# Kernel optimization log

Hardware: AMD Instinct MI355X
Metric: run time of the kernel (lower is better)

Reference implementation:

```python
import jax, jax.numpy as jnp
import numpy as np

B = 512          # batch
T_STEPS = 32     # clip_length (loop runs T-1 = 32 times)
BELIEF = 1024
STATE = 256
HIDDEN = 1024
EMB = 1024
POSE_TILES = 1
MIN_STD = 0.1


def setup_inputs() -> dict:
    key = jax.random.key(0)
    ks = jax.random.split(key, 24)
    s = 0.02
    rn = lambda k, sh: (jax.random.normal(k, sh, dtype=jnp.float32) * s)
    d = {
        "prev_state": jax.random.normal(ks[0], (B, STATE), dtype=jnp.float32),
        "prev_belief": jax.random.normal(ks[1], (B, BELIEF), dtype=jnp.float32),
        "poses": jax.random.normal(ks[2], (T_STEPS, B, 6), dtype=jnp.float32),
        "observations": jax.random.normal(ks[3], (T_STEPS, B, EMB), dtype=jnp.float32),
        "post_noise": jax.random.normal(ks[4], (T_STEPS, B, STATE), dtype=jnp.float32),
        "prior_noise": jax.random.normal(ks[5], (T_STEPS, B, STATE), dtype=jnp.float32),
        # fc_embed_state: 2*state -> belief
        "w_es": rn(ks[6], (2 * STATE, BELIEF)), "b_es": jnp.zeros((BELIEF,), jnp.float32),
        # GRUCell(belief, belief); torch gate order r, z, n
        "w_ih": rn(ks[7], (BELIEF, 3 * BELIEF)), "w_hh": rn(ks[8], (BELIEF, 3 * BELIEF)),
        "b_ih": jnp.zeros((3 * BELIEF,), jnp.float32), "b_hh": jnp.zeros((3 * BELIEF,), jnp.float32),
        # fc_embed_belief_posterior: belief+emb -> hidden
        "w_ebpo": rn(ks[9], (BELIEF + EMB, HIDDEN)), "b_ebpo": jnp.zeros((HIDDEN,), jnp.float32),
        # fc_state_posterior: hidden -> 2*state
        "w_spo": rn(ks[10], (HIDDEN, 2 * STATE)), "b_spo": jnp.zeros((2 * STATE,), jnp.float32),
        # fc_embed_belief_prior: belief + 6*pose_tiles -> hidden
        "w_ebpr": rn(ks[11], (BELIEF + 6 * POSE_TILES, HIDDEN)), "b_ebpr": jnp.zeros((HIDDEN,), jnp.float32),
        # fc_state_prior: hidden -> 2*state
        "w_spr": rn(ks[12], (HIDDEN, 2 * STATE)), "b_spr": jnp.zeros((2 * STATE,), jnp.float32),
    }
    return d


def _rssm(prev_state, prev_belief, poses, observations, post_noise, prior_noise,
          w_es, b_es, w_ih, w_hh, b_ih, b_hh,
          w_ebpo, b_ebpo, w_spo, b_spo, w_ebpr, b_ebpr, w_spr, b_spr):
    def gru_cell(x, h):
        gi = x @ w_ih + b_ih
        gh = h @ w_hh + b_hh
        ir, iz, inn = jnp.split(gi, 3, axis=1)
        hr, hz, hn = jnp.split(gh, 3, axis=1)
        r = jax.nn.sigmoid(ir + hr)
        z = jax.nn.sigmoid(iz + hz)
        n = jnp.tanh(inn + r * hn)
        return (1.0 - z) * n + z * h

    def step(carry, xs):
        post_s, prior_s, belief = carry
        obs_t, pose_t, n_post, n_prior = xs
        hidden = jax.nn.relu(jnp.concatenate([post_s, prior_s], axis=1) @ w_es + b_es)
        belief = gru_cell(hidden, belief)
        # posterior branch
        hp = jax.nn.relu(jnp.concatenate([belief, obs_t], axis=1) @ w_ebpo + b_ebpo)
        pm, psd_raw = jnp.split(hp @ w_spo + b_spo, 2, axis=1)
        psd = jax.nn.softplus(psd_raw) + MIN_STD
        ps = pm + psd * n_post
        # prior branch (pose tiled)
        pose_rep = jnp.tile(pose_t, (1, POSE_TILES))
        hq = jax.nn.relu(jnp.concatenate([belief, pose_rep], axis=1) @ w_ebpr + b_ebpr)
        prm, prsd_raw = jnp.split(hq @ w_spr + b_spr, 2, axis=1)
        prsd = jax.nn.softplus(prsd_raw) + MIN_STD
        prs = prm + prsd * n_prior
        return (ps, prs, belief), (belief, prs, prm, prsd, ps, pm, psd)

    init = (prev_state, prev_state, prev_belief)
    _, outs = jax.lax.scan(step, init, (observations, poses, post_noise, prior_noise))
    # outs: beliefs, prior_states, prior_means, prior_std_devs, posterior_states, posterior_means, posterior_std_devs  (each [T-1, B, *])
    return outs


def reference(prev_state, prev_belief, poses, observations, post_noise, prior_noise,
              w_es, b_es, w_ih, w_hh, b_ih, b_hh,
              w_ebpo, b_ebpo, w_spo, b_spo, w_ebpr, b_ebpr, w_spr, b_spr):
    return _rssm(prev_state, prev_belief, poses, observations, post_noise, prior_noise,
                 w_es, b_es, w_ih, w_hh, b_ih, b_hh,
                 w_ebpo, b_ebpo, w_spo, b_spo, w_ebpr, b_ebpr, w_spr, b_spr)
```

## Files before the change

kernel.cpp:

```cpp
#include <hip/hip_runtime.h>
#include <math.h>


typedef __attribute__((ext_vector_type(8))) short bf16x8;
typedef __attribute__((ext_vector_type(4))) float f32x4;

#define MFMA(a, b, c) __builtin_amdgcn_mfma_f32_16x16x32_bf16(a, b, c, 0, 0, 0)

__device__ __forceinline__ short f2bf(float f) {
    unsigned u = __float_as_uint(f);
    u += 0x7FFF + ((u >> 16) & 1);
    return (short)(u >> 16);
}
__device__ __forceinline__ float sigmoidf_(float x) { return 1.f / (1.f + expf(-x)); }
__device__ __forceinline__ float softplusf_(float x) {
    return fmaxf(x, 0.f) + log1pf(expf(-fabsf(x)));
}
__device__ __forceinline__ f32x4 zero4() { f32x4 v = {0.f, 0.f, 0.f, 0.f}; return v; }

__global__ __launch_bounds__(256) void k_swizzle(const float* __restrict__ W,
                                                 short* __restrict__ out,
                                                 int KT, int N)
{
    int gw = blockIdx.x * 4 + (threadIdx.x >> 6);
    int lane = threadIdx.x & 63;
    int nt = gw / KT, kt = gw % KT;
    const float* src = W + (size_t)(kt * 32 + (lane >> 4) * 8) * N + nt * 16 + (lane & 15);
    short tmp[8];
#pragma unroll
    for (int j = 0; j < 8; ++j) tmp[j] = f2bf(src[(size_t)j * N]);
    *(bf16x8*)(out + (((size_t)gw * 64 + lane) << 3)) = *(const bf16x8*)tmp;
}

__global__ __launch_bounds__(256) void k_obs2bf(const float* __restrict__ obs,
                                                short* __restrict__ out)
{
    size_t i = ((size_t)blockIdx.x * 256 + threadIdx.x) * 8;
    short tmp[8];
#pragma unroll
    for (int j = 0; j < 8; ++j) tmp[j] = f2bf(obs[i + j]);
    *(bf16x8*)(out + i) = *(const bf16x8*)tmp;
}

__global__ __launch_bounds__(256) void k_init(const float* __restrict__ prev_state,
                                              const float* __restrict__ prev_belief,
                                              short* __restrict__ stateCat,
                                              short* __restrict__ belief1)
{
    int i = blockIdx.x * 256 + threadIdx.x;
    if (i < 262144) {
        int m = i >> 9, c = i & 511;
        stateCat[i] = f2bf(prev_state[m * 256 + (c & 255)]);
    } else {
        int j = i - 262144;
        belief1[j] = f2bf(prev_belief[j]);
    }
}

__device__ __forceinline__ bf16x8 loadA16(const short* A, int m0, int kelem, int strideElems, int lane) {
    return *(const bf16x8*)(A + (size_t)(m0 + (lane & 15)) * strideElems + kelem + ((lane >> 4) << 3));
}
__device__ __forceinline__ bf16x8 loadB16(const short* Bsw, size_t tileIdx, int lane) {
    return *(const bf16x8*)(Bsw + ((tileIdx * 64 + lane) << 3));
}

__global__ __launch_bounds__(256) void k_embed_state(
    const short* __restrict__ A, const short* __restrict__ Bsw,
    const float* __restrict__ bias, short* __restrict__ outBf)
{
    int wid = threadIdx.x >> 6;
    int lane = threadIdx.x & 63;
    int nt = blockIdx.x & 63, mb = blockIdx.x >> 6;
    int m0 = (mb * 4 + wid) * 32;
    f32x4 acc0 = zero4(), acc1 = zero4();
#pragma unroll 4
    for (int kt = 0; kt < 16; ++kt) {
        bf16x8 a0 = loadA16(A, m0,      kt * 32, 512, lane);
        bf16x8 a1 = loadA16(A, m0 + 16, kt * 32, 512, lane);
        bf16x8 b  = loadB16(Bsw, (size_t)nt * 16 + kt, lane);
        acc0 = MFMA(a0, b, acc0);
        acc1 = MFMA(a1, b, acc1);
    }
    int q = lane >> 4, cl = lane & 15;
    int n = nt * 16 + cl;
    float bn = bias[n];
#pragma unroll
    for (int i = 0; i < 4; ++i) {
        int m = m0 + q * 4 + i;
        outBf[(size_t)m * 1024 + n]        = f2bf(fmaxf(acc0[i] + bn, 0.f));
        outBf[(size_t)(m + 16) * 1024 + n] = f2bf(fmaxf(acc1[i] + bn, 0.f));
    }
}

__global__ __launch_bounds__(256) void k_gru(
    const short* __restrict__ Hbf, const short* __restrict__ Pbf,
    const float* __restrict__ Pf32,
    const short* __restrict__ sw_ih, const short* __restrict__ sw_hh,
    const float* __restrict__ b_ih, const float* __restrict__ b_hh,
    float* __restrict__ belF32, short* __restrict__ belBf)
{
    int wid = threadIdx.x >> 6;
    int lane = threadIdx.x & 63;
    int nt = blockIdx.x & 63, mb = blockIdx.x >> 6;
    int m0 = (mb * 4 + wid) * 32;
    f32x4 r0 = zero4(), r1 = zero4(), z0 = zero4(), z1 = zero4();
    f32x4 ni0 = zero4(), ni1 = zero4(), nh0 = zero4(), nh1 = zero4();

#pragma unroll 4
    for (int kt = 0; kt < 32; ++kt) {
        bf16x8 a0 = loadA16(Hbf, m0,      kt * 32, 1024, lane);
        bf16x8 a1 = loadA16(Hbf, m0 + 16, kt * 32, 1024, lane);
        bf16x8 br = loadB16(sw_ih, (size_t)(0 * 64 + nt) * 32 + kt, lane);
        bf16x8 bz = loadB16(sw_ih, (size_t)(1 * 64 + nt) * 32 + kt, lane);
        bf16x8 bn = loadB16(sw_ih, (size_t)(2 * 64 + nt) * 32 + kt, lane);
        r0 = MFMA(a0, br, r0);   r1 = MFMA(a1, br, r1);
        z0 = MFMA(a0, bz, z0);   z1 = MFMA(a1, bz, z1);
        ni0 = MFMA(a0, bn, ni0); ni1 = MFMA(a1, bn, ni1);
    }
#pragma unroll 4
    for (int kt = 0; kt < 32; ++kt) {
        bf16x8 a0 = loadA16(Pbf, m0,      kt * 32, 1024, lane);
        bf16x8 a1 = loadA16(Pbf, m0 + 16, kt * 32, 1024, lane);
        bf16x8 br = loadB16(sw_hh, (size_t)(0 * 64 + nt) * 32 + kt, lane);
        bf16x8 bz = loadB16(sw_hh, (size_t)(1 * 64 + nt) * 32 + kt, lane);
        bf16x8 bn = loadB16(sw_hh, (size_t)(2 * 64 + nt) * 32 + kt, lane);
        r0 = MFMA(a0, br, r0);   r1 = MFMA(a1, br, r1);
        z0 = MFMA(a0, bz, z0);   z1 = MFMA(a1, bz, z1);
        nh0 = MFMA(a0, bn, nh0); nh1 = MFMA(a1, bn, nh1);
    }

    int q = lane >> 4, cl = lane & 15;
    int n = nt * 16 + cl;
    float bihr = b_ih[n] + b_hh[n];
    float bihz = b_ih[1024 + n] + b_hh[1024 + n];
    float bin = b_ih[2048 + n], bhn = b_hh[2048 + n];
#pragma unroll
    for (int f = 0; f < 2; ++f) {
#pragma unroll
        for (int i = 0; i < 4; ++i) {
            int m = m0 + f * 16 + q * 4 + i;
            float rv = f ? r1[i] : r0[i];
            float zv = f ? z1[i] : z0[i];
            float niv = f ? ni1[i] : ni0[i];
            float nhv = f ? nh1[i] : nh0[i];
            float rr = sigmoidf_(rv + bihr);
            float zz = sigmoidf_(zv + bihz);
            float ng = tanhf(niv + bin + rr * (nhv + bhn));
            float h = Pf32[(size_t)m * 1024 + n];
            float v = (1.f - zz) * ng + zz * h;
            belF32[(size_t)m * 1024 + n] = v;
            belBf[(size_t)m * 1024 + n] = f2bf(v);
        }
    }
}

__global__ __launch_bounds__(256) void k_pp(
    const short* __restrict__ Bel, const short* __restrict__ ObsBf,
    const float* __restrict__ Pose,
    const short* __restrict__ sw_ebpo, const short* __restrict__ sw_ebpr,
    const float* __restrict__ Wf_ebpr,
    const float* __restrict__ b_ebpo, const float* __restrict__ b_ebpr,
    short* __restrict__ hpBf, short* __restrict__ hqBf)
{
    int wid = threadIdx.x >> 6;
    int lane = threadIdx.x & 63;
    int q = lane >> 4, cl = lane & 15;
    int b = blockIdx.x;
    if (b < 256) {
        int nt = b & 63, mb = b >> 6;
        int m0 = (mb * 4 + wid) * 32;
        f32x4 acc0 = zero4(), acc1 = zero4();
#pragma unroll 4
        for (int kt = 0; kt < 32; ++kt) {
            bf16x8 a0 = loadA16(Bel, m0,      kt * 32, 1024, lane);
            bf16x8 a1 = loadA16(Bel, m0 + 16, kt * 32, 1024, lane);
            bf16x8 bb = loadB16(sw_ebpo, (size_t)nt * 64 + kt, lane);
            acc0 = MFMA(a0, bb, acc0);
            acc1 = MFMA(a1, bb, acc1);
        }
#pragma unroll 4
        for (int kt = 32; kt < 64; ++kt) {
            bf16x8 a0 = loadA16(ObsBf, m0,      (kt - 32) * 32, 1024, lane);
            bf16x8 a1 = loadA16(ObsBf, m0 + 16, (kt - 32) * 32, 1024, lane);
            bf16x8 bb = loadB16(sw_ebpo, (size_t)nt * 64 + kt, lane);
            acc0 = MFMA(a0, bb, acc0);
            acc1 = MFMA(a1, bb, acc1);
        }
        int n = nt * 16 + cl;
        float bn = b_ebpo[n];
#pragma unroll
        for (int i = 0; i < 4; ++i) {
            int m = m0 + q * 4 + i;
            hpBf[(size_t)m * 1024 + n]        = f2bf(fmaxf(acc0[i] + bn, 0.f));
            hpBf[(size_t)(m + 16) * 1024 + n] = f2bf(fmaxf(acc1[i] + bn, 0.f));
        }
    } else {
        int b2 = b - 256;
        int nt = b2 & 63, mb = b2 >> 6;
        int m0 = (mb * 4 + wid) * 32;
        f32x4 acc0 = zero4(), acc1 = zero4();
#pragma unroll 4
        for (int kt = 0; kt < 32; ++kt) {
            bf16x8 a0 = loadA16(Bel, m0,      kt * 32, 1024, lane);
            bf16x8 a1 = loadA16(Bel, m0 + 16, kt * 32, 1024, lane);
            bf16x8 bb = loadB16(sw_ebpr, (size_t)nt * 32 + kt, lane);
            acc0 = MFMA(a0, bb, acc0);
            acc1 = MFMA(a1, bb, acc1);
        }
        int n = nt * 16 + cl;
        float bn = b_ebpr[n];
#pragma unroll
        for (int f = 0; f < 2; ++f) {
#pragma unroll
            for (int i = 0; i < 4; ++i) {
                int m = m0 + f * 16 + q * 4 + i;
                float v = (f ? acc1[i] : acc0[i]) + bn;
#pragma unroll
                for (int p = 0; p < 6; ++p)
                    v += Pose[(size_t)m * 6 + p] * Wf_ebpr[(size_t)(1024 + p) * 1024 + n];
                hqBf[(size_t)m * 1024 + n] = f2bf(fmaxf(v, 0.f));
            }
        }
    }
}

__global__ __launch_bounds__(256) void k_head(
    const short* __restrict__ Hp, const short* __restrict__ Hq,
    const short* __restrict__ sw_spo, const short* __restrict__ sw_spr,
    const float* __restrict__ b_spo, const float* __restrict__ b_spr,
    const float* __restrict__ nPost, const float* __restrict__ nPri,
    float* __restrict__ pM, float* __restrict__ pS, float* __restrict__ pSt,
    float* __restrict__ qM, float* __restrict__ qS, float* __restrict__ qSt,
    short* __restrict__ stateCat)
{
    int gw = blockIdx.x * 4 + (threadIdx.x >> 6);
    int lane = threadIdx.x & 63;
    int br = gw >> 9, rem = gw & 511;
    int mt = rem >> 4, ct = rem & 15;
    int m0 = mt * 16;
    const short* A = br ? Hq : Hp;
    const short* Bsw = br ? sw_spr : sw_spo;
    const float* bias = br ? b_spr : b_spo;
    const float* noise = br ? nPri : nPost;
    float* mO = br ? qM : pM;
    float* sO = br ? qS : pS;
    float* stO = br ? qSt : pSt;
    int catOff = br ? 256 : 0;
    f32x4 ma = zero4(), sa = zero4();
#pragma unroll 4
    for (int kt = 0; kt < 32; ++kt) {
        bf16x8 a = loadA16(A, m0, kt * 32, 1024, lane);
        bf16x8 bm = loadB16(Bsw, (size_t)ct * 32 + kt, lane);
        bf16x8 bs = loadB16(Bsw, (size_t)(16 + ct) * 32 + kt, lane);
        ma = MFMA(a, bm, ma);
        sa = MFMA(a, bs, sa);
    }
    int q = lane >> 4, cl = lane & 15;
#pragma unroll
    for (int i = 0; i < 4; ++i) {
        int m = m0 + q * 4 + i;
        int c = ct * 16 + cl;
        float mean = ma[i] + bias[c];
        float sd = softplusf_(sa[i] + bias[c + 256]) + 0.1f;
        float st = mean + sd * noise[(size_t)m * 256 + c];
        mO[(size_t)m * 256 + c] = mean;
        sO[(size_t)m * 256 + c] = sd;
        stO[(size_t)m * 256 + c] = st;
        stateCat[(size_t)m * 512 + catOff + c] = f2bf(st);
    }
}

extern "C" void kernel_launch(void* const* d_in, const int* in_sizes, int n_in,
                              void* d_out, int out_size, void* d_ws, size_t ws_size,
                              hipStream_t stream)
{
    const float* prev_state  = (const float*)d_in[0];
    const float* prev_belief = (const float*)d_in[1];
    const float* poses       = (const float*)d_in[2];
    const float* obs         = (const float*)d_in[3];
    const float* post_noise  = (const float*)d_in[4];
    const float* prior_noise = (const float*)d_in[5];
    const float* w_es   = (const float*)d_in[6];
    const float* b_es   = (const float*)d_in[7];
    const float* w_ih   = (const float*)d_in[8];
    const float* w_hh   = (const float*)d_in[9];
    const float* b_ih   = (const float*)d_in[10];
    const float* b_hh   = (const float*)d_in[11];
    const float* w_ebpo = (const float*)d_in[12];
    const float* b_ebpo = (const float*)d_in[13];
    const float* w_spo  = (const float*)d_in[14];
    const float* b_spo  = (const float*)d_in[15];
    const float* w_ebpr = (const float*)d_in[16];
    const float* b_ebpr = (const float*)d_in[17];
    const float* w_spr  = (const float*)d_in[18];
    const float* b_spr  = (const float*)d_in[19];

    float* out = (float*)d_out;
    float* beliefs    = out;
    float* priStates  = out + 16777216;
    float* priMeans   = out + 20971520;
    float* priStds    = out + 25165824;
    float* postStates = out + 29360128;
    float* postMeans  = out + 33554432;
    float* postStds   = out + 37748736;

    short* ws = (short*)d_ws;
    size_t o = 0;
    short* sw_es   = ws + o; o += (size_t)512 * 1024;
    short* sw_ih   = ws + o; o += (size_t)1024 * 3072;
    short* sw_hh   = ws + o; o += (size_t)1024 * 3072;
    short* sw_ebpo = ws + o; o += (size_t)2048 * 1024;
    short* sw_ebpr = ws + o; o += (size_t)1024 * 1024;
    short* sw_spo  = ws + o; o += (size_t)1024 * 512;
    short* sw_spr  = ws + o; o += (size_t)1024 * 512;
    short* hidden  = ws + o; o += (size_t)512 * 1024;
    short* belBuf0 = ws + o; o += (size_t)512 * 1024;
    short* belBuf1 = ws + o; o += (size_t)512 * 1024;
    short* hpBuf   = ws + o; o += (size_t)512 * 1024;
    short* hqBuf   = ws + o; o += (size_t)512 * 1024;
    short* stateCat = ws + o; o += (size_t)512 * 512;
    short* obsBf   = ws + o; o += (size_t)32 * 512 * 1024;

    k_swizzle<<<dim3(256),  dim3(256), 0, stream>>>(w_es,   sw_es,   16, 1024);
    k_swizzle<<<dim3(1536), dim3(256), 0, stream>>>(w_ih,   sw_ih,   32, 3072);
    k_swizzle<<<dim3(1536), dim3(256), 0, stream>>>(w_hh,   sw_hh,   32, 3072);
    k_swizzle<<<dim3(1024), dim3(256), 0, stream>>>(w_ebpo, sw_ebpo, 64, 1024);
    k_swizzle<<<dim3(512),  dim3(256), 0, stream>>>(w_ebpr, sw_ebpr, 32, 1024);
    k_swizzle<<<dim3(256),  dim3(256), 0, stream>>>(w_spo,  sw_spo,  32, 512);
    k_swizzle<<<dim3(256),  dim3(256), 0, stream>>>(w_spr,  sw_spr,  32, 512);
    k_obs2bf<<<dim3(8192), dim3(256), 0, stream>>>(obs, obsBf);
    k_init<<<dim3(3072), dim3(256), 0, stream>>>(prev_state, prev_belief, stateCat, belBuf1);

    for (int t = 0; t < 32; ++t) {
        short* belPrevBf = (t & 1) ? belBuf0 : belBuf1;
        short* belCurBf  = (t & 1) ? belBuf1 : belBuf0;
        const float* belPrevF = t ? (beliefs + (size_t)(t - 1) * 524288) : prev_belief;
        float* belT = beliefs + (size_t)t * 524288;

        k_embed_state<<<dim3(256), dim3(256), 0, stream>>>(stateCat, sw_es, b_es, hidden);
        k_gru<<<dim3(256), dim3(256), 0, stream>>>(hidden, belPrevBf, belPrevF,
                                                   sw_ih, sw_hh, b_ih, b_hh, belT, belCurBf);
        k_pp<<<dim3(512), dim3(256), 0, stream>>>(belCurBf, obsBf + (size_t)t * 524288,
                                                  poses + (size_t)t * 3072,
                                                  sw_ebpo, sw_ebpr, w_ebpr,
                                                  b_ebpo, b_ebpr, hpBuf, hqBuf);
        k_head<<<dim3(256), dim3(256), 0, stream>>>(hpBuf, hqBuf, sw_spo, sw_spr, b_spo, b_spr,
                                                    post_noise + (size_t)t * 131072,
                                                    prior_noise + (size_t)t * 131072,
                                                    postMeans + (size_t)t * 131072,
                                                    postStds + (size_t)t * 131072,
                                                    postStates + (size_t)t * 131072,
                                                    priMeans + (size_t)t * 131072,
                                                    priStds + (size_t)t * 131072,
                                                    priStates + (size_t)t * 131072,
                                                    stateCat);
    }
}
```

Baseline: 2.693 ms.

## Fuse per-step kernels into one persistent cooperative kernel with grid barriers

Replaces the 128 per-timestep kernel launches with a single cooperative persistent kernel of 256 blocks. It loops over time steps and separates the embed, GRU, posterior/prior hidden and head phases with a software global barrier built on atomics. This removes launch and drain overhead between dependent phases. The trade-off is that the k_pp phase, which previously used 512 blocks, now runs serially within 256 blocks, and the spin barriers add their own latency. The old multi-launch path is kept as a fallback if the cooperative launch fails.

```diff
diff --git a/kernel.cpp b/kernel.cpp
--- a/kernel.cpp
+++ b/kernel.cpp
@@ -45,9 +45,11 @@
 __global__ __launch_bounds__(256) void k_init(const float* __restrict__ prev_state,
                                               const float* __restrict__ prev_belief,
                                               short* __restrict__ stateCat,
-                                              short* __restrict__ belief1)
+                                              short* __restrict__ belief1,
+                                              unsigned* __restrict__ bar)
 {
     int i = blockIdx.x * 256 + threadIdx.x;
+    if (i == 0) { bar[0] = 0u; bar[1] = 0u; }
     if (i < 262144) {
         int m = i >> 9, c = i & 511;
         stateCat[i] = f2bf(prev_state[m * 256 + (c & 255)]);
@@ -64,6 +66,215 @@
     return *(const bf16x8*)(Bsw + ((tileIdx * 64 + lane) << 3));
 }
 
+#define NBLK 256
+
+__device__ __forceinline__ void gbar(unsigned* bar)
+{
+    __syncthreads();
+    if (threadIdx.x == 0) {
+        __threadfence();
+        unsigned g = __hip_atomic_load(bar + 1, __ATOMIC_RELAXED, __HIP_MEMORY_SCOPE_AGENT);
+        unsigned a = __hip_atomic_fetch_add(bar, 1u, __ATOMIC_ACQ_REL, __HIP_MEMORY_SCOPE_AGENT);
+        if (a == NBLK - 1) {
+            __hip_atomic_store(bar, 0u, __ATOMIC_RELAXED, __HIP_MEMORY_SCOPE_AGENT);
+            __hip_atomic_fetch_add(bar + 1, 1u, __ATOMIC_RELEASE, __HIP_MEMORY_SCOPE_AGENT);
+        } else {
+            while (__hip_atomic_load(bar + 1, __ATOMIC_ACQUIRE, __HIP_MEMORY_SCOPE_AGENT) == g)
+                __builtin_amdgcn_s_sleep(2);
+        }
+        __threadfence();
+    }
+    __syncthreads();
+}
+
+struct RP {
+    const short *sw_es, *sw_ih, *sw_hh, *sw_ebpo, *sw_ebpr, *sw_spo, *sw_spr;
+    const float *Wf_ebpr;
+    const float *b_es, *b_ih, *b_hh, *b_ebpo, *b_ebpr, *b_spo, *b_spr;
+    const float *prev_belief, *poses, *post_noise, *prior_noise;
+    const short *obsBf;
+    short *hidden, *belBuf0, *belBuf1, *hpBuf, *hqBuf, *stateCat;
+    float *beliefs, *priStates, *priMeans, *priStds, *postStates, *postMeans, *postStds;
+    unsigned *bar;
+};
+
+__global__ __launch_bounds__(256, 1) void k_rssm(RP p)
+{
+    int wid = threadIdx.x >> 6;
+    int lane = threadIdx.x & 63;
+    int q = lane >> 4, cl = lane & 15;
+    int nt = blockIdx.x & 63, mb = blockIdx.x >> 6;
+    int m0 = (mb * 4 + wid) * 32;
+
+#pragma unroll 1
+    for (int t = 0; t < 32; ++t) {
+        {
+            f32x4 acc0 = zero4(), acc1 = zero4();
+#pragma unroll 4
+            for (int kt = 0; kt < 16; ++kt) {
+                bf16x8 a0 = loadA16(p.stateCat, m0,      kt * 32, 512, lane);
+                bf16x8 a1 = loadA16(p.stateCat, m0 + 16, kt * 32, 512, lane);
+                bf16x8 b  = loadB16(p.sw_es, (size_t)nt * 16 + kt, lane);
+                acc0 = MFMA(a0, b, acc0);
+                acc1 = MFMA(a1, b, acc1);
+            }
+            int n = nt * 16 + cl;
+            float bn = p.b_es[n];
+#pragma unroll
+            for (int i = 0; i < 4; ++i) {
+                int m = m0 + q * 4 + i;
+                p.hidden[(size_t)m * 1024 + n]        = f2bf(fmaxf(acc0[i] + bn, 0.f));
+                p.hidden[(size_t)(m + 16) * 1024 + n] = f2bf(fmaxf(acc1[i] + bn, 0.f));
+            }
+        }
+        gbar(p.bar);
+
+        const short* belPrevBf = (t & 1) ? p.belBuf0 : p.belBuf1;
+        short* belCurBf        = (t & 1) ? p.belBuf1 : p.belBuf0;
+        const float* Pf32 = t ? (p.beliefs + (size_t)(t - 1) * 524288) : p.prev_belief;
+        float* belT = p.beliefs + (size_t)t * 524288;
+        {
+            f32x4 r0 = zero4(), r1 = zero4(), z0 = zero4(), z1 = zero4();
+            f32x4 ni0 = zero4(), ni1 = zero4(), nh0 = zero4(), nh1 = zero4();
+#pragma unroll 4
+            for (int kt = 0; kt < 32; ++kt) {
+                bf16x8 a0 = loadA16(p.hidden, m0,      kt * 32, 1024, lane);
+                bf16x8 a1 = loadA16(p.hidden, m0 + 16, kt * 32, 1024, lane);
+                bf16x8 br = loadB16(p.sw_ih, (size_t)(0 * 64 + nt) * 32 + kt, lane);
+                bf16x8 bz = loadB16(p.sw_ih, (size_t)(1 * 64 + nt) * 32 + kt, lane);
+                bf16x8 bn = loadB16(p.sw_ih, (size_t)(2 * 64 + nt) * 32 + kt, lane);
+                r0 = MFMA(a0, br, r0);   r1 = MFMA(a1, br, r1);
+                z0 = MFMA(a0, bz, z0);   z1 = MFMA(a1, bz, z1);
+                ni0 = MFMA(a0, bn, ni0); ni1 = MFMA(a1, bn, ni1);
+            }
+#pragma unroll 4
+            for (int kt = 0; kt < 32; ++kt) {
+                bf16x8 a0 = loadA16(belPrevBf, m0,      kt * 32, 1024, lane);
+                bf16x8 a1 = loadA16(belPrevBf, m0 + 16, kt * 32, 1024, lane);
+                bf16x8 br = loadB16(p.sw_hh, (size_t)(0 * 64 + nt) * 32 + kt, lane);
+                bf16x8 bz = loadB16(p.sw_hh, (size_t)(1 * 64 + nt) * 32 + kt, lane);
+                bf16x8 bn = loadB16(p.sw_hh, (size_t)(2 * 64 + nt) * 32 + kt, lane);
+                r0 = MFMA(a0, br, r0);   r1 = MFMA(a1, br, r1);
+                z0 = MFMA(a0, bz, z0);   z1 = MFMA(a1, bz, z1);
+                nh0 = MFMA(a0, bn, nh0); nh1 = MFMA(a1, bn, nh1);
+            }
+            int n = nt * 16 + cl;
+            float bihr = p.b_ih[n] + p.b_hh[n];
+            float bihz = p.b_ih[1024 + n] + p.b_hh[1024 + n];
+            float bin = p.b_ih[2048 + n], bhn = p.b_hh[2048 + n];
+#pragma unroll
+            for (int f = 0; f < 2; ++f) {
+#pragma unroll
+                for (int i = 0; i < 4; ++i) {
+                    int m = m0 + f * 16 + q * 4 + i;
+                    float rv = f ? r1[i] : r0[i];
+                    float zv = f ? z1[i] : z0[i];
+                    float niv = f ? ni1[i] : ni0[i];
+                    float nhv = f ? nh1[i] : nh0[i];
+                    float rr = sigmoidf_(rv + bihr);
+                    float zz = sigmoidf_(zv + bihz);
+                    float ng = tanhf(niv + bin + rr * (nhv + bhn));
+                    float h = Pf32[(size_t)m * 1024 + n];
+                    float v = (1.f - zz) * ng + zz * h;
+                    belT[(size_t)m * 1024 + n] = v;
+                    belCurBf[(size_t)m * 1024 + n] = f2bf(v);
+                }
+            }
+        }
+        gbar(p.bar);
+
+        const short* obsT = p.obsBf + (size_t)t * 524288;
+        const float* poseT = p.poses + (size_t)t * 3072;
+        {
+            f32x4 acc0 = zero4(), acc1 = zero4();
+#pragma unroll 4
+            for (int kt = 0; kt < 32; ++kt) {
+                bf16x8 a0 = loadA16(belCurBf, m0,      kt * 32, 1024, lane);
+                bf16x8 a1 = loadA16(belCurBf, m0 + 16, kt * 32, 1024, lane);
+                bf16x8 bb = loadB16(p.sw_ebpo, (size_t)nt * 64 + kt, lane);
+                acc0 = MFMA(a0, bb, acc0);
+                acc1 = MFMA(a1, bb, acc1);
+            }
+#pragma unroll 4
+            for (int kt = 32; kt < 64; ++kt) {
+                bf16x8 a0 = loadA16(obsT, m0,      (kt - 32) * 32, 1024, lane);
+                bf16x8 a1 = loadA16(obsT, m0 + 16, (kt - 32) * 32, 1024, lane);
+                bf16x8 bb = loadB16(p.sw_ebpo, (size_t)nt * 64 + kt, lane);
+                acc0 = MFMA(a0, bb, acc0);
+                acc1 = MFMA(a1, bb, acc1);
+            }
+            int n = nt * 16 + cl;
+            float bn = p.b_ebpo[n];
+#pragma unroll
+            for (int i = 0; i < 4; ++i) {
+                int m = m0 + q * 4 + i;
+                p.hpBuf[(size_t)m * 1024 + n]        = f2bf(fmaxf(acc0[i] + bn, 0.f));
+                p.hpBuf[(size_t)(m + 16) * 1024 + n] = f2bf(fmaxf(acc1[i] + bn, 0.f));
+            }
+            acc0 = zero4(); acc1 = zero4();
+#pragma unroll 4
+            for (int kt = 0; kt < 32; ++kt) {
+                bf16x8 a0 = loadA16(belCurBf, m0,      kt * 32, 1024, lane);
+                bf16x8 a1 = loadA16(belCurBf, m0 + 16, kt * 32, 1024, lane);
+                bf16x8 bb = loadB16(p.sw_ebpr, (size_t)nt * 32 + kt, lane);
+                acc0 = MFMA(a0, bb, acc0);
+                acc1 = MFMA(a1, bb, acc1);
+            }
+            float bn2 = p.b_ebpr[n];
+#pragma unroll
+            for (int f = 0; f < 2; ++f) {
+#pragma unroll
+                for (int i = 0; i < 4; ++i) {
+                    int m = m0 + f * 16 + q * 4 + i;
+                    float v = (f ? acc1[i] : acc0[i]) + bn2;
+#pragma unroll
+                    for (int pp = 0; pp < 6; ++pp)
+                        v += poseT[(size_t)m * 6 + pp] * p.Wf_ebpr[(size_t)(1024 + pp) * 1024 + n];
+                    p.hqBuf[(size_t)m * 1024 + n] = f2bf(fmaxf(v, 0.f));
+                }
+            }
+        }
+        gbar(p.bar);
+
+        {
+            int gw = blockIdx.x * 4 + wid;
+            int br = gw >> 9, rem = gw & 511;
+            int mt = rem >> 4, ct = rem & 15;
+            int mh = mt * 16;
+            const short* A = br ? p.hqBuf : p.hpBuf;
+            const short* Bsw = br ? p.sw_spr : p.sw_spo;
+            const float* bias = br ? p.b_spr : p.b_spo;
+            const float* noise = (br ? p.prior_noise : p.post_noise) + (size_t)t * 131072;
+            float* mO  = (br ? p.priMeans  : p.postMeans)  + (size_t)t * 131072;
+            float* sO  = (br ? p.priStds   : p.postStds)   + (size_t)t * 131072;
+            float* stO = (br ? p.priStates : p.postStates) + (size_t)t * 131072;
+            int catOff = br ? 256 : 0;
+            f32x4 ma = zero4(), sa = zero4();
+#pragma unroll 4
+            for (int kt = 0; kt < 32; ++kt) {
+                bf16x8 a = loadA16(A, mh, kt * 32, 1024, lane);
+                bf16x8 bm = loadB16(Bsw, (size_t)ct * 32 + kt, lane);
+                bf16x8 bs = loadB16(Bsw, (size_t)(16 + ct) * 32 + kt, lane);
+                ma = MFMA(a, bm, ma);
+                sa = MFMA(a, bs, sa);
+            }
+#pragma unroll
+            for (int i = 0; i < 4; ++i) {
+                int m = mh + q * 4 + i;
+                int c = ct * 16 + cl;
+                float mean = ma[i] + bias[c];
+                float sd = softplusf_(sa[i] + bias[c + 256]) + 0.1f;
+                float st = mean + sd * noise[(size_t)m * 256 + c];
+                mO[(size_t)m * 256 + c] = mean;
+                sO[(size_t)m * 256 + c] = sd;
+                stO[(size_t)m * 256 + c] = st;
+                p.stateCat[(size_t)m * 512 + catOff + c] = f2bf(st);
+            }
+        }
+        gbar(p.bar);
+    }
+}
+
 __global__ __launch_bounds__(256) void k_embed_state(
     const short* __restrict__ A, const short* __restrict__ Bsw,
     const float* __restrict__ bias, short* __restrict__ outBf)
@@ -105,7 +316,6 @@
     int m0 = (mb * 4 + wid) * 32;
     f32x4 r0 = zero4(), r1 = zero4(), z0 = zero4(), z1 = zero4();
     f32x4 ni0 = zero4(), ni1 = zero4(), nh0 = zero4(), nh1 = zero4();
-
 #pragma unroll 4
     for (int kt = 0; kt < 32; ++kt) {
         bf16x8 a0 = loadA16(Hbf, m0,      kt * 32, 1024, lane);
@@ -128,7 +338,6 @@
         z0 = MFMA(a0, bz, z0);   z1 = MFMA(a1, bz, z1);
         nh0 = MFMA(a0, bn, nh0); nh1 = MFMA(a1, bn, nh1);
     }
-
     int q = lane >> 4, cl = lane & 15;
     int n = nt * 16 + cl;
     float bihr = b_ih[n] + b_hh[n];
@@ -216,8 +425,8 @@
                 int m = m0 + f * 16 + q * 4 + i;
                 float v = (f ? acc1[i] : acc0[i]) + bn;
 #pragma unroll
-                for (int p = 0; p < 6; ++p)
-                    v += Pose[(size_t)m * 6 + p] * Wf_ebpr[(size_t)(1024 + p) * 1024 + n];
+                for (int pp = 0; pp < 6; ++pp)
+                    v += Pose[(size_t)m * 6 + pp] * Wf_ebpr[(size_t)(1024 + pp) * 1024 + n];
                 hqBf[(size_t)m * 1024 + n] = f2bf(fmaxf(v, 0.f));
             }
         }
@@ -320,6 +529,7 @@
     short* hqBuf   = ws + o; o += (size_t)512 * 1024;
     short* stateCat = ws + o; o += (size_t)512 * 512;
     short* obsBf   = ws + o; o += (size_t)32 * 512 * 1024;
+    unsigned* bar  = (unsigned*)(ws + o); o += 8;
 
     k_swizzle<<<dim3(256),  dim3(256), 0, stream>>>(w_es,   sw_es,   16, 1024);
     k_swizzle<<<dim3(1536), dim3(256), 0, stream>>>(w_ih,   sw_ih,   32, 3072);
@@ -329,30 +539,51 @@
     k_swizzle<<<dim3(256),  dim3(256), 0, stream>>>(w_spo,  sw_spo,  32, 512);
     k_swizzle<<<dim3(256),  dim3(256), 0, stream>>>(w_spr,  sw_spr,  32, 512);
     k_obs2bf<<<dim3(8192), dim3(256), 0, stream>>>(obs, obsBf);
-    k_init<<<dim3(3072), dim3(256), 0, stream>>>(prev_state, prev_belief, stateCat, belBuf1);
-
-    for (int t = 0; t < 32; ++t) {
-        short* belPrevBf = (t & 1) ? belBuf0 : belBuf1;
-        short* belCurBf  = (t & 1) ? belBuf1 : belBuf0;
-        const float* belPrevF = t ? (beliefs + (size_t)(t - 1) * 524288) : prev_belief;
-        float* belT = beliefs + (size_t)t * 524288;
-
-        k_embed_state<<<dim3(256), dim3(256), 0, stream>>>(stateCat, sw_es, b_es, hidden);
-        k_gru<<<dim3(256), dim3(256), 0, stream>>>(hidden, belPrevBf, belPrevF,
-                                                   sw_ih, sw_hh, b_ih, b_hh, belT, belCurBf);
-        k_pp<<<dim3(512), dim3(256), 0, stream>>>(belCurBf, obsBf + (size_t)t * 524288,
-                                                  poses + (size_t)t * 3072,
-                                                  sw_ebpo, sw_ebpr, w_ebpr,
-                                                  b_ebpo, b_ebpr, hpBuf, hqBuf);
-        k_head<<<dim3(256), dim3(256), 0, stream>>>(hpBuf, hqBuf, sw_spo, sw_spr, b_spo, b_spr,
-                                                    post_noise + (size_t)t * 131072,
-                                                    prior_noise + (size_t)t * 131072,
-                                                    postMeans + (size_t)t * 131072,
-                                                    postStds + (size_t)t * 131072,
-                                                    postStates + (size_t)t * 131072,
-                                                    priMeans + (size_t)t * 131072,
-                                                    priStds + (size_t)t * 131072,
-                                                    priStates + (size_t)t * 131072,
-                                                    stateCat);
-    }
-}
+    k_init<<<dim3(3072), dim3(256), 0, stream>>>(prev_state, prev_belief, stateCat, belBuf1, bar);
+
+    RP rp;
+    rp.sw_es = sw_es; rp.sw_ih = sw_ih; rp.sw_hh = sw_hh;
+    rp.sw_ebpo = sw_ebpo; rp.sw_ebpr = sw_ebpr; rp.sw_spo = sw_spo; rp.sw_spr = sw_spr;
+    rp.Wf_ebpr = w_ebpr;
+    rp.b_es = b_es; rp.b_ih = b_ih; rp.b_hh = b_hh;
+    rp.b_ebpo = b_ebpo; rp.b_ebpr = b_ebpr; rp.b_spo = b_spo; rp.b_spr = b_spr;
+    rp.prev_belief = prev_belief; rp.poses = poses;
+    rp.post_noise = post_noise; rp.prior_noise = prior_noise;
+    rp.obsBf = obsBf;
+    rp.hidden = hidden; rp.belBuf0 = belBuf0; rp.belBuf1 = belBuf1;
+    rp.hpBuf = hpBuf; rp.hqBuf = hqBuf; rp.stateCat = stateCat;
+    rp.beliefs = beliefs;
+    rp.priStates = priStates; rp.priMeans = priMeans; rp.priStds = priStds;
+    rp.postStates = postStates; rp.postMeans = postMeans; rp.postStds = postStds;
+    rp.bar = bar;
+
+    void* kargs[] = { (void*)&rp };
+    hipError_t ce = hipLaunchCooperativeKernel(k_rssm, dim3(NBLK), dim3(256),
+                                               kargs, 0u, stream);
+    if (ce != hipSuccess) {
+        for (int t = 0; t < 32; ++t) {
+            short* belPrevBf = (t & 1) ? belBuf0 : belBuf1;
+            short* belCurBf  = (t & 1) ? belBuf1 : belBuf0;
+            const float* belPrevF = t ? (beliefs + (size_t)(t - 1) * 524288) : prev_belief;
+            float* belT = beliefs + (size_t)t * 524288;
+
+            k_embed_state<<<dim3(256), dim3(256), 0, stream>>>(stateCat, sw_es, b_es, hidden);
+            k_gru<<<dim3(256), dim3(256), 0, stream>>>(hidden, belPrevBf, belPrevF,
+                                                       sw_ih, sw_hh, b_ih, b_hh, belT, belCurBf);
+            k_pp<<<dim3(512), dim3(256), 0, stream>>>(belCurBf, obsBf + (size_t)t * 524288,
+                                                      poses + (size_t)t * 3072,
+                                                      sw_ebpo, sw_ebpr, w_ebpr,
+                                                      b_ebpo, b_ebpr, hpBuf, hqBuf);
+            k_head<<<dim3(256), dim3(256), 0, stream>>>(hpBuf, hqBuf, sw_spo, sw_spr, b_spo, b_spr,
+                                                        post_noise + (size_t)t * 131072,
+                                                        prior_noise + (size_t)t * 131072,
+                                                        postMeans + (size_t)t * 131072,
+                                                        postStds + (size_t)t * 131072,
+                                                        postStates + (size_t)t * 131072,
+                                                        priMeans + (size_t)t * 131072,
+                                                        priStds + (size_t)t * 131072,
+                                                        priStates + (size_t)t * 131072,
+                                                        stateCat);
+        }
+    }
+}
```

Measured after the change: 6.485 ms. 2.41x slower.
